# Performance work log

Measured on AMD Instinct MI355X. Metric: run time of the kernel, lower is better.

The kernel has to match this reference:

```python
import jax, jax.numpy as jnp
import numpy as np

B, N, DIM = 4, 2048, 1024
H, DH = 16, 64


def setup_inputs() -> dict:
    key = jax.random.key(0)
    k1, k2, k3 = jax.random.split(key, 3)
    x = jax.random.normal(k1, (B, N, DIM), dtype=jnp.float32)
    # nn.Linear weight layout: [out_features, in_features]; y = x @ W.T
    w_qkv = jax.random.normal(k2, (3 * H * DH, DIM), dtype=jnp.float32) * (DIM ** -0.5)
    w_out = jax.random.normal(k3, (DIM, H * DH), dtype=jnp.float32) * ((H * DH) ** -0.5)
    b_out = jnp.zeros((DIM,), dtype=jnp.float32)
    return {"x": x, "w_qkv": w_qkv, "w_out": w_out, "b_out": b_out}


def reference(x, w_qkv, w_out, b_out):
    scale = DH ** -0.5
    qkv = jnp.einsum('bnd,ed->bne', x, w_qkv)            # [B,N,3*H*DH]
    q, k, v = jnp.split(qkv, 3, axis=-1)
    def to_heads(t):
        return t.reshape(B, N, H, DH).transpose(0, 2, 1, 3)  # b h n d
    q, k, v = to_heads(q), to_heads(k), to_heads(v)
    scores = jnp.einsum('bhnd,bhmd->bhnm', q, k) * scale  # [B,H,N,N]
    att = jax.nn.softmax(scores, axis=-1)
    out = jnp.einsum('bhnm,bhmd->bhnd', att, v)
    out = out.transpose(0, 2, 1, 3).reshape(B, N, H * DH)  # b n (h d)
    return jnp.einsum('bne,de->bnd', out, w_out) + b_out
```

## Files before the change

kernel.cpp:

```cpp
#include <hip/hip_runtime.h>
#include <hip/hip_bf16.h>
#include <math.h>

#define B_   4
#define N_   2048
#define DIM_ 1024
#define H_   16
#define DH_  64
#define E3_  3072

typedef __attribute__((ext_vector_type(8)))  short s8v;
typedef __attribute__((ext_vector_type(4)))  float f4v;
typedef __attribute__((ext_vector_type(16))) float f16v;

__device__ __forceinline__ unsigned short f2bf_fast(float f) {
    return (unsigned short)((__builtin_bit_cast(unsigned int, f) + 0x8000u) >> 16);
}
__device__ __forceinline__ unsigned int pkbf(float a, float b) {
    unsigned int ua = __builtin_bit_cast(unsigned int, a) + 0x8000u;
    unsigned int ub = __builtin_bit_cast(unsigned int, b) + 0x8000u;
    return __builtin_amdgcn_perm(ub, ua, 0x07060302);
}
__device__ __forceinline__ unsigned int cvtpk(float a, float b) {
    unsigned int r;
    asm("v_cvt_pk_bf16_f32 %0, %1, %2" : "=v"(r) : "v"(a), "v"(b));
    return r;
}
__device__ __forceinline__ uint2 pl32(unsigned int a, unsigned int b) {
    asm volatile("v_permlane32_swap_b32 %0, %1" : "+v"(a), "+v"(b));
    return make_uint2(a, b);
}

__device__ __forceinline__ void gload_lds16(const void* g, void* l) {
    __builtin_amdgcn_global_load_lds(
        (const __attribute__((address_space(1))) unsigned int*)(uintptr_t)g,
        (__attribute__((address_space(3))) unsigned int*)(uintptr_t)l,
        16, 0, 0);
}

__global__ __launch_bounds__(256) void cvt_bf16(
    const float* __restrict__ in, unsigned short* __restrict__ out, int n)
{
    const int i = (blockIdx.x * 256 + threadIdx.x) * 4;
    if (i < n) {
        float4 v = *(const float4*)(in + i);
        uint2 pk;
        pk.x = pkbf(v.x, v.y);
        pk.y = pkbf(v.z, v.w);
        *(uint2*)(out + i) = pk;
    }
}

template<int MODE>
__global__ __launch_bounds__(256) void gemm_mfma(
    const unsigned short* __restrict__ A,
    const unsigned short* __restrict__ Bw,
    const float* __restrict__ bias,
    unsigned short* __restrict__ Cb,
    unsigned short* __restrict__ Vt,
    float* __restrict__ Cf,
    int M, int Nc, int K)
{
    __shared__ unsigned short As[128 * 32];
    __shared__ unsigned short Bs[128 * 32];

    const int tid  = threadIdx.x;
    const int w    = tid >> 6;
    const int lane = tid & 63;
    const int quad = lane >> 4;
    const int l15  = lane & 15;
    const int wm   = w & 1, wn = w >> 1;
    const int m0   = blockIdx.y * 128, n0 = blockIdx.x * 128;

    const int srow = lane >> 2;
    const int sch  = (lane & 3) * 8;

    f4v acc[4][4];
    #pragma unroll
    for (int i = 0; i < 4; i++)
        #pragma unroll
        for (int j = 0; j < 4; j++) acc[i][j] = (f4v){0.f, 0.f, 0.f, 0.f};

    for (int k0 = 0; k0 < K; k0 += 32) {
        __syncthreads();
        #pragma unroll
        for (int i = 0; i < 2; i++) {
            const int rbase = w * 32 + i * 16;
            gload_lds16(A  + (size_t)(m0 + rbase + srow) * K + k0 + sch,
                        &As[rbase * 32]);
            gload_lds16(Bw + (size_t)(n0 + rbase + srow) * K + k0 + sch,
                        &Bs[rbase * 32]);
        }
        __syncthreads();

        s8v af[4], bf[4];
        #pragma unroll
        for (int i = 0; i < 4; i++) {
            af[i] = *(const s8v*)&As[(wm * 64 + i * 16 + l15) * 32 + quad * 8];
            bf[i] = *(const s8v*)&Bs[(wn * 64 + i * 16 + l15) * 32 + quad * 8];
        }
        #pragma unroll
        for (int ms = 0; ms < 4; ms++)
            #pragma unroll
            for (int ns = 0; ns < 4; ns++)
                acc[ms][ns] = __builtin_amdgcn_mfma_f32_16x16x32_bf16(
                    af[ms], bf[ns], acc[ms][ns], 0, 0, 0);
    }

    if (MODE == 0) {
        #pragma unroll
        for (int ns = 0; ns < 4; ns++) {
            const int colb = n0 + wn * 64 + ns * 16;
            if (colb < 2048) {
                const float mul = (colb < 1024) ? 0.18033688011112042f : 1.0f;
                #pragma unroll
                for (int ms = 0; ms < 4; ms++)
                    #pragma unroll
                    for (int r = 0; r < 4; r++) {
                        const int row = m0 + wm * 64 + ms * 16 + quad * 4 + r;
                        Cb[(size_t)row * Nc + colb + l15] = f2bf_fast(acc[ms][ns][r] * mul);
                    }
            } else {
                const int e = colb + l15 - 2048;
                const int h = e >> 6, d = e & 63;
                #pragma unroll
                for (int ms = 0; ms < 4; ms++) {
                    const int row = m0 + wm * 64 + ms * 16 + quad * 4;
                    const int b = row >> 11, n = row & 2047;
                    uint2 pk;
                    pk.x = pkbf(acc[ms][ns][0], acc[ms][ns][1]);
                    pk.y = pkbf(acc[ms][ns][2], acc[ms][ns][3]);
                    *(uint2*)&Vt[(((size_t)b * 16 + h) * 64 + d) * 2048 + n] = pk;
                }
            }
        }
    } else {
        #pragma unroll
        for (int ns = 0; ns < 4; ns++) {
            const float bz = bias[n0 + wn * 64 + ns * 16 + l15];
            #pragma unroll
            for (int ms = 0; ms < 4; ms++)
                #pragma unroll
                for (int r = 0; r < 4; r++) {
                    const int row = m0 + wm * 64 + ms * 16 + quad * 4 + r;
                    Cf[(size_t)row * Nc + n0 + wn * 64 + ns * 16 + l15] =
                        acc[ms][ns][r] + bz;
                }
        }
    }
}

__global__ __launch_bounds__(256, 2) void attn_mfma(
    const unsigned short* __restrict__ qkv,
    const unsigned short* __restrict__ vT,
    unsigned short* __restrict__ ao)
{
    __shared__ __align__(16) unsigned short Ks[2][64][64];
    __shared__ __align__(16) unsigned short Vs[2][64][64];

    const int tid  = threadIdx.x;
    const int w    = tid >> 6;
    const int lane = tid & 63;
    const int l31  = lane & 31;
    const int hi5  = lane >> 5;
    const int h8   = hi5 * 8;

    const int bh = blockIdx.y;
    const int b  = bh >> 4;
    const int h  = bh & 15;
    const int q0 = blockIdx.x * 256;

    const unsigned short* qp  = qkv + (size_t)b * N_ * E3_ + (size_t)h * DH_;
    const unsigned short* kp  = qp + 1024;
    const unsigned short* vtp = vT + (size_t)bh * 64 * 2048;

    const int srow0 = tid >> 3;
    const int srow1 = srow0 + 32;
    const int sc    = tid & 7;
    const int sw0   = (sc ^ (srow0 & 7)) * 8;
    const int sw1   = (sc ^ (srow1 & 7)) * 8;

    s8v bq[2][4];
    #pragma unroll
    for (int sub = 0; sub < 2; sub++) {
        const unsigned short* qrow =
            qp + (size_t)(q0 + w * 64 + sub * 32 + l31) * E3_;
        #pragma unroll
        for (int ks = 0; ks < 4; ks++)
            bq[sub][ks] = *(const s8v*)(qrow + ks * 16 + h8);
    }

    s8v ones;
    #pragma unroll
    for (int i = 0; i < 8; i++) ones[i] = (short)0x3F80;

    const f16v fzero = {0.f,0.f,0.f,0.f,0.f,0.f,0.f,0.f,
                        0.f,0.f,0.f,0.f,0.f,0.f,0.f,0.f};
    f16v o[2][2];
    o[0][0] = fzero; o[0][1] = fzero; o[1][0] = fzero; o[1][1] = fzero;
    f16v lc[2];
    lc[0] = fzero; lc[1] = fzero;

    {
        s8v k0 = *(const s8v*)(kp  + (size_t)srow0 * E3_  + sc * 8);
        s8v k1 = *(const s8v*)(kp  + (size_t)srow1 * E3_  + sc * 8);
        s8v v0 = *(const s8v*)(vtp + (size_t)srow0 * 2048 + sc * 8);
        s8v v1 = *(const s8v*)(vtp + (size_t)srow1 * 2048 + sc * 8);
        *(s8v*)&Ks[0][srow0][sw0] = k0;
        *(s8v*)&Ks[0][srow1][sw1] = k1;
        *(s8v*)&Vs[0][srow0][sw0] = v0;
        *(s8v*)&Vs[0][srow1][sw1] = v1;
    }
    __syncthreads();

    for (int kt = 0; kt < N_ / 64; kt++) {
        const int cur = kt & 1;
        const bool pre = (kt + 1 < N_ / 64);

        s8v pk0, pk1, pv0, pv1;
        if (pre) {
            const int kn = (kt + 1) * 64;
            pk0 = *(const s8v*)(kp  + (size_t)(kn + srow0) * E3_ + sc * 8);
            pk1 = *(const s8v*)(kp  + (size_t)(kn + srow1) * E3_ + sc * 8);
            pv0 = *(const s8v*)(vtp + (size_t)srow0 * 2048 + kn + sc * 8);
            pv1 = *(const s8v*)(vtp + (size_t)srow1 * 2048 + kn + sc * 8);
        }

        #pragma unroll
        for (int ksub = 0; ksub < 2; ksub++) {
            const int krow = ksub * 32 + l31;
            const int ksw  = (krow & 7) * 8;
            s8v ak[4];
            #pragma unroll
            for (int ks = 0; ks < 4; ks++)
                ak[ks] = *(const s8v*)&Ks[cur][krow][(ks * 16 + h8) ^ ksw];

            s8v pa[2][2];
            #pragma unroll
            for (int sub = 0; sub < 2; sub++) {
                f16v st = fzero;
                __builtin_amdgcn_s_setprio(1);
                st = __builtin_amdgcn_mfma_f32_32x32x16_bf16(ak[0], bq[sub][0], st, 0, 0, 0);
                st = __builtin_amdgcn_mfma_f32_32x32x16_bf16(ak[1], bq[sub][1], st, 0, 0, 0);
                st = __builtin_amdgcn_mfma_f32_32x32x16_bf16(ak[2], bq[sub][2], st, 0, 0, 0);
                st = __builtin_amdgcn_mfma_f32_32x32x16_bf16(ak[3], bq[sub][3], st, 0, 0, 0);
                __builtin_amdgcn_s_setprio(0);

                float pe[16];
                #pragma unroll
                for (int i = 0; i < 16; i++)
                    pe[i] = __builtin_amdgcn_exp2f(st[i]);

                union { s8v v; unsigned int u[4]; } f0, f1;
                uint2 r;
                r = pl32(cvtpk(pe[0],  pe[1]),  cvtpk(pe[4],  pe[5]));
                f0.u[0] = r.x; f0.u[2] = r.y;
                r = pl32(cvtpk(pe[2],  pe[3]),  cvtpk(pe[6],  pe[7]));
                f0.u[1] = r.x; f0.u[3] = r.y;
                r = pl32(cvtpk(pe[8],  pe[9]),  cvtpk(pe[12], pe[13]));
                f1.u[0] = r.x; f1.u[2] = r.y;
                r = pl32(cvtpk(pe[10], pe[11]), cvtpk(pe[14], pe[15]));
                f1.u[1] = r.x; f1.u[3] = r.y;
                pa[sub][0] = f0.v;
                pa[sub][1] = f1.v;
            }

            #pragma unroll
            for (int j = 0; j < 2; j++) {
                const int kbase = (ksub * 2 + j) * 16 + h8;
                const int vsw   = (l31 & 7) * 8;
                s8v bv0 = *(const s8v*)&Vs[cur][l31     ][kbase ^ vsw];
                s8v bv1 = *(const s8v*)&Vs[cur][32 + l31][kbase ^ vsw];
                __builtin_amdgcn_s_setprio(1);
                o[0][0] = __builtin_amdgcn_mfma_f32_32x32x16_bf16(pa[0][j], bv0, o[0][0], 0, 0, 0);
                o[1][0] = __builtin_amdgcn_mfma_f32_32x32x16_bf16(pa[1][j], bv0, o[1][0], 0, 0, 0);
                o[0][1] = __builtin_amdgcn_mfma_f32_32x32x16_bf16(pa[0][j], bv1, o[0][1], 0, 0, 0);
                o[1][1] = __builtin_amdgcn_mfma_f32_32x32x16_bf16(pa[1][j], bv1, o[1][1], 0, 0, 0);
                lc[0]   = __builtin_amdgcn_mfma_f32_32x32x16_bf16(pa[0][j], ones, lc[0], 0, 0, 0);
                lc[1]   = __builtin_amdgcn_mfma_f32_32x32x16_bf16(pa[1][j], ones, lc[1], 0, 0, 0);
                __builtin_amdgcn_s_setprio(0);
            }
        }

        if (pre) {
            const int nxt = cur ^ 1;
            *(s8v*)&Ks[nxt][srow0][sw0] = pk0;
            *(s8v*)&Ks[nxt][srow1][sw1] = pk1;
            *(s8v*)&Vs[nxt][srow0][sw0] = pv0;
            *(s8v*)&Vs[nxt][srow1][sw1] = pv1;
        }
        __syncthreads();
    }

    #pragma unroll
    for (int sub = 0; sub < 2; sub++) {
        float inv[16];
        #pragma unroll
        for (int r = 0; r < 16; r++) inv[r] = 1.f / lc[sub][r];
        #pragma unroll
        for (int dt = 0; dt < 2; dt++)
            #pragma unroll
            for (int r = 0; r < 16; r++) {
                const int qrow = q0 + w * 64 + sub * 32 + (r & 3) + 8 * (r >> 2) + 4 * hi5;
                ao[((size_t)b * N_ + qrow) * (H_ * DH_) + h * DH_ + dt * 32 + l31] =
                    f2bf_fast(o[sub][dt][r] * inv[r]);
            }
    }
}

extern "C" void kernel_launch(void* const* d_in, const int* in_sizes, int n_in,
                              void* d_out, int out_size, void* d_ws, size_t ws_size,
                              hipStream_t stream) {
    const float* x     = (const float*)d_in[0];
    const float* w_qkv = (const float*)d_in[1];
    const float* w_out = (const float*)d_in[2];
    const float* b_out = (const float*)d_in[3];
    float* out = (float*)d_out;

    char* ws = (char*)d_ws;
    unsigned short* x_bf    = (unsigned short*)(ws);
    unsigned short* wqkv_bf = (unsigned short*)(ws + (((size_t)16) << 20));
    unsigned short* wout_bf = (unsigned short*)(ws + (((size_t)22) << 20));
    unsigned short* qkv_bf  = (unsigned short*)(ws + (((size_t)24) << 20));
    unsigned short* vT      = (unsigned short*)(ws + (((size_t)72) << 20));
    unsigned short* ao_bf   = (unsigned short*)(ws + (((size_t)88) << 20));

    const int M = B_ * N_;

    cvt_bf16<<<(M * DIM_) / 1024, 256, 0, stream>>>(x, x_bf, M * DIM_);
    cvt_bf16<<<(E3_ * DIM_) / 1024, 256, 0, stream>>>(w_qkv, wqkv_bf, E3_ * DIM_);
    cvt_bf16<<<(DIM_ * DIM_) / 1024, 256, 0, stream>>>(w_out, wout_bf, DIM_ * DIM_);

    {
        dim3 grid(E3_ / 128, M / 128);
        gemm_mfma<0><<<grid, 256, 0, stream>>>(x_bf, wqkv_bf, nullptr,
                                               qkv_bf, vT, nullptr, M, E3_, DIM_);
    }
    {
        dim3 grid(N_ / 256, B_ * H_);
        attn_mfma<<<grid, 256, 0, stream>>>(qkv_bf, vT, ao_bf);
    }
    {
        dim3 grid(DIM_ / 128, M / 128);
        gemm_mfma<1><<<grid, 256, 0, stream>>>(ao_bf, wout_bf, b_out,
                                               nullptr, nullptr, out, M, DIM_, DIM_);
    }
    (void)in_sizes; (void)n_in; (void)out_size; (void)ws_size;
}
```

Baseline: 285.3 us.

## Widen attention blocks to 8 waves, use direct-to-LDS loads, swizzle block order

The attention kernel moves from 4 waves of 64 query rows each to 8 waves of 32 query rows each, which halves the per-wave accumulator registers and targets higher occupancy. K/V tiles are now staged with direct global-to-LDS loads instead of register round-trips. Block indices in both the GEMM and attention kernels are remapped (XCD-style swizzle) so neighbouring blocks share K/V or weight tiles in cache. The trade-off is that each K tile read from LDS is reused for fewer query rows, and the swizzle assumes the block count divides evenly by 8.

Result: faster. 276.3 us (-3.1%).

```diff
diff --git a/kernel.cpp b/kernel.cpp
--- a/kernel.cpp
+++ b/kernel.cpp
@@ -70,7 +70,12 @@
     const int quad = lane >> 4;
     const int l15  = lane & 15;
     const int wm   = w & 1, wn = w >> 1;
-    const int m0   = blockIdx.y * 128, n0 = blockIdx.x * 128;
+
+    const int nwx = gridDim.x;
+    const int lin = blockIdx.y * nwx + blockIdx.x;
+    const int cpx = (nwx * gridDim.y) >> 3;
+    const int swz = (lin & 7) * cpx + (lin >> 3);
+    const int m0  = (swz / nwx) * 128, n0 = (swz % nwx) * 128;
 
     const int srow = lane >> 2;
     const int sch  = (lane & 3) * 8;
@@ -150,7 +155,7 @@
     }
 }
 
-__global__ __launch_bounds__(256, 2) void attn_mfma(
+__global__ __launch_bounds__(512, 4) void attn_mfma(
     const unsigned short* __restrict__ qkv,
     const unsigned short* __restrict__ vT,
     unsigned short* __restrict__ ao)
@@ -165,29 +170,29 @@
     const int hi5  = lane >> 5;
     const int h8   = hi5 * 8;
 
-    const int bh = blockIdx.y;
-    const int b  = bh >> 4;
-    const int h  = bh & 15;
-    const int q0 = blockIdx.x * 256;
+    const int lin = blockIdx.y * 8 + blockIdx.x;
+    const int swz = (lin & 7) * 64 + (lin >> 3);
+    const int bx  = swz & 7;
+    const int bh  = swz >> 3;
+    const int b   = bh >> 4;
+    const int h   = bh & 15;
+    const int q0  = bx * 256;
+    const int qb  = q0 + w * 32;
 
     const unsigned short* qp  = qkv + (size_t)b * N_ * E3_ + (size_t)h * DH_;
     const unsigned short* kp  = qp + 1024;
     const unsigned short* vtp = vT + (size_t)bh * 64 * 2048;
 
-    const int srow0 = tid >> 3;
-    const int srow1 = srow0 + 32;
-    const int sc    = tid & 7;
-    const int sw0   = (sc ^ (srow0 & 7)) * 8;
-    const int sw1   = (sc ^ (srow1 & 7)) * 8;
-
-    s8v bq[2][4];
-    #pragma unroll
-    for (int sub = 0; sub < 2; sub++) {
-        const unsigned short* qrow =
-            qp + (size_t)(q0 + w * 64 + sub * 32 + l31) * E3_;
+    const int drow = lane >> 3;
+    const int dchk = (lane & 7) ^ drow;
+    const int grow = w * 8 + drow;
+
+    s8v bq[4];
+    {
+        const unsigned short* qrow = qp + (size_t)(qb + l31) * E3_;
         #pragma unroll
         for (int ks = 0; ks < 4; ks++)
-            bq[sub][ks] = *(const s8v*)(qrow + ks * 16 + h8);
+            bq[ks] = *(const s8v*)(qrow + ks * 16 + h8);
     }
 
     s8v ones;
@@ -196,61 +201,48 @@
 
     const f16v fzero = {0.f,0.f,0.f,0.f,0.f,0.f,0.f,0.f,
                         0.f,0.f,0.f,0.f,0.f,0.f,0.f,0.f};
-    f16v o[2][2];
-    o[0][0] = fzero; o[0][1] = fzero; o[1][0] = fzero; o[1][1] = fzero;
-    f16v lc[2];
-    lc[0] = fzero; lc[1] = fzero;
-
-    {
-        s8v k0 = *(const s8v*)(kp  + (size_t)srow0 * E3_  + sc * 8);
-        s8v k1 = *(const s8v*)(kp  + (size_t)srow1 * E3_  + sc * 8);
-        s8v v0 = *(const s8v*)(vtp + (size_t)srow0 * 2048 + sc * 8);
-        s8v v1 = *(const s8v*)(vtp + (size_t)srow1 * 2048 + sc * 8);
-        *(s8v*)&Ks[0][srow0][sw0] = k0;
-        *(s8v*)&Ks[0][srow1][sw1] = k1;
-        *(s8v*)&Vs[0][srow0][sw0] = v0;
-        *(s8v*)&Vs[0][srow1][sw1] = v1;
-    }
+    f16v o0 = fzero, o1 = fzero;
+    f16v lc = fzero;
+
+    gload_lds16(kp  + (size_t)grow * E3_  + dchk * 8, &Ks[0][w * 8][0]);
+    gload_lds16(vtp + (size_t)grow * 2048 + dchk * 8, &Vs[0][w * 8][0]);
     __syncthreads();
 
     for (int kt = 0; kt < N_ / 64; kt++) {
         const int cur = kt & 1;
-        const bool pre = (kt + 1 < N_ / 64);
-
-        s8v pk0, pk1, pv0, pv1;
-        if (pre) {
+
+        if (kt + 1 < N_ / 64) {
             const int kn = (kt + 1) * 64;
-            pk0 = *(const s8v*)(kp  + (size_t)(kn + srow0) * E3_ + sc * 8);
-            pk1 = *(const s8v*)(kp  + (size_t)(kn + srow1) * E3_ + sc * 8);
-            pv0 = *(const s8v*)(vtp + (size_t)srow0 * 2048 + kn + sc * 8);
-            pv1 = *(const s8v*)(vtp + (size_t)srow1 * 2048 + kn + sc * 8);
+            gload_lds16(kp  + (size_t)(kn + grow) * E3_  + dchk * 8,
+                        &Ks[cur ^ 1][w * 8][0]);
+            gload_lds16(vtp + (size_t)grow * 2048 + kn + dchk * 8,
+                        &Vs[cur ^ 1][w * 8][0]);
         }
 
         #pragma unroll
         for (int ksub = 0; ksub < 2; ksub++) {
             const int krow = ksub * 32 + l31;
-            const int ksw  = (krow & 7) * 8;
+            const int ksw  = (l31 & 7) * 8;
             s8v ak[4];
             #pragma unroll
             for (int ks = 0; ks < 4; ks++)
                 ak[ks] = *(const s8v*)&Ks[cur][krow][(ks * 16 + h8) ^ ksw];
 
-            s8v pa[2][2];
-            #pragma unroll
-            for (int sub = 0; sub < 2; sub++) {
-                f16v st = fzero;
-                __builtin_amdgcn_s_setprio(1);
-                st = __builtin_amdgcn_mfma_f32_32x32x16_bf16(ak[0], bq[sub][0], st, 0, 0, 0);
-                st = __builtin_amdgcn_mfma_f32_32x32x16_bf16(ak[1], bq[sub][1], st, 0, 0, 0);
-                st = __builtin_amdgcn_mfma_f32_32x32x16_bf16(ak[2], bq[sub][2], st, 0, 0, 0);
-                st = __builtin_amdgcn_mfma_f32_32x32x16_bf16(ak[3], bq[sub][3], st, 0, 0, 0);
-                __builtin_amdgcn_s_setprio(0);
-
-                float pe[16];
-                #pragma unroll
-                for (int i = 0; i < 16; i++)
-                    pe[i] = __builtin_amdgcn_exp2f(st[i]);
-
+            f16v st = fzero;
+            __builtin_amdgcn_s_setprio(1);
+            st = __builtin_amdgcn_mfma_f32_32x32x16_bf16(ak[0], bq[0], st, 0, 0, 0);
+            st = __builtin_amdgcn_mfma_f32_32x32x16_bf16(ak[1], bq[1], st, 0, 0, 0);
+            st = __builtin_amdgcn_mfma_f32_32x32x16_bf16(ak[2], bq[2], st, 0, 0, 0);
+            st = __builtin_amdgcn_mfma_f32_32x32x16_bf16(ak[3], bq[3], st, 0, 0, 0);
+            __builtin_amdgcn_s_setprio(0);
+
+            float pe[16];
+            #pragma unroll
+            for (int i = 0; i < 16; i++)
+                pe[i] = __builtin_amdgcn_exp2f(st[i]);
+
+            s8v pa[2];
+            {
                 union { s8v v; unsigned int u[4]; } f0, f1;
                 uint2 r;
                 r = pl32(cvtpk(pe[0],  pe[1]),  cvtpk(pe[4],  pe[5]));
@@ -261,8 +253,8 @@
                 f1.u[0] = r.x; f1.u[2] = r.y;
                 r = pl32(cvtpk(pe[10], pe[11]), cvtpk(pe[14], pe[15]));
                 f1.u[1] = r.x; f1.u[3] = r.y;
-                pa[sub][0] = f0.v;
-                pa[sub][1] = f1.v;
+                pa[0] = f0.v;
+                pa[1] = f1.v;
             }
 
             #pragma unroll
@@ -272,39 +264,27 @@
                 s8v bv0 = *(const s8v*)&Vs[cur][l31     ][kbase ^ vsw];
                 s8v bv1 = *(const s8v*)&Vs[cur][32 + l31][kbase ^ vsw];
                 __builtin_amdgcn_s_setprio(1);
-                o[0][0] = __builtin_amdgcn_mfma_f32_32x32x16_bf16(pa[0][j], bv0, o[0][0], 0, 0, 0);
-                o[1][0] = __builtin_amdgcn_mfma_f32_32x32x16_bf16(pa[1][j], bv0, o[1][0], 0, 0, 0);
-                o[0][1] = __builtin_amdgcn_mfma_f32_32x32x16_bf16(pa[0][j], bv1, o[0][1], 0, 0, 0);
-                o[1][1] = __builtin_amdgcn_mfma_f32_32x32x16_bf16(pa[1][j], bv1, o[1][1], 0, 0, 0);
-                lc[0]   = __builtin_amdgcn_mfma_f32_32x32x16_bf16(pa[0][j], ones, lc[0], 0, 0, 0);
-                lc[1]   = __builtin_amdgcn_mfma_f32_32x32x16_bf16(pa[1][j], ones, lc[1], 0, 0, 0);
+                o0 = __builtin_amdgcn_mfma_f32_32x32x16_bf16(pa[j], bv0, o0, 0, 0, 0);
+                o1 = __builtin_amdgcn_mfma_f32_32x32x16_bf16(pa[j], bv1, o1, 0, 0, 0);
+                lc = __builtin_amdgcn_mfma_f32_32x32x16_bf16(pa[j], ones, lc, 0, 0, 0);
                 __builtin_amdgcn_s_setprio(0);
             }
         }
 
-        if (pre) {
-            const int nxt = cur ^ 1;
-            *(s8v*)&Ks[nxt][srow0][sw0] = pk0;
-            *(s8v*)&Ks[nxt][srow1][sw1] = pk1;
-            *(s8v*)&Vs[nxt][srow0][sw0] = pv0;
-            *(s8v*)&Vs[nxt][srow1][sw1] = pv1;
-        }
         __syncthreads();
     }
 
-    #pragma unroll
-    for (int sub = 0; sub < 2; sub++) {
+    {
         float inv[16];
         #pragma unroll
-        for (int r = 0; r < 16; r++) inv[r] = 1.f / lc[sub][r];
-        #pragma unroll
-        for (int dt = 0; dt < 2; dt++)
-            #pragma unroll
-            for (int r = 0; r < 16; r++) {
-                const int qrow = q0 + w * 64 + sub * 32 + (r & 3) + 8 * (r >> 2) + 4 * hi5;
-                ao[((size_t)b * N_ + qrow) * (H_ * DH_) + h * DH_ + dt * 32 + l31] =
-                    f2bf_fast(o[sub][dt][r] * inv[r]);
-            }
+        for (int r = 0; r < 16; r++) inv[r] = 1.f / lc[r];
+        #pragma unroll
+        for (int r = 0; r < 16; r++) {
+            const int qrow = qb + (r & 3) + 8 * (r >> 2) + 4 * hi5;
+            const size_t base = ((size_t)b * N_ + qrow) * (H_ * DH_) + h * DH_;
+            ao[base + l31]      = f2bf_fast(o0[r] * inv[r]);
+            ao[base + 32 + l31] = f2bf_fast(o1[r] * inv[r]);
+        }
     }
 }
 
@@ -338,7 +318,7 @@
     }
     {
         dim3 grid(N_ / 256, B_ * H_);
-        attn_mfma<<<grid, 256, 0, stream>>>(qkv_bf, vT, ao_bf);
+        attn_mfma<<<grid, 512, 0, stream>>>(qkv_bf, vT, ao_bf);
     }
     {
         dim3 grid(DIM_ / 128, M / 128);
```
